# Kernel optimization log

Hardware: AMD Instinct MI355X
Metric: run time of the kernel (lower is better)

## Reference

```python
import jax, jax.numpy as jnp
import numpy as np

R = 3                      # corr_radius
K = (2 * R + 1) ** 2       # 49 correlation window
BANDS = 16
MAX_FREQ = 512.0
NUM_ITERS = 4
EPS = 1e-5


def _fourier(coords):
    # coords [..., D] -> [..., D*(2*BANDS+1)]
    freqs = (2.0 ** jnp.linspace(0.0, np.log2(MAX_FREQ), BANDS).astype(coords.dtype)) * np.pi
    x = coords[..., None] * freqs                      # [..., D, BANDS]
    enc = jnp.concatenate([jnp.sin(x), jnp.cos(x)], axis=-1)
    enc = enc.reshape(enc.shape[:-2] + (-1,))
    return jnp.concatenate([coords, enc], axis=-1)


def _layernorm(x, g, b):
    m = jnp.mean(x, -1, keepdims=True)
    v = jnp.mean(jnp.square(x - m), -1, keepdims=True)
    return (x - m) * jax.lax.rsqrt(v + EPS) * g + b


def _local_corr(query, fmaps, positions, stride):
    # query [B,Q,C], fmaps [B,T,C,H,W], positions [B,Q,T,2] -> corr [B,Q,T,K]
    B, T, C, H, W = fmaps.shape
    Q = query.shape[1]
    off = jnp.arange(-R, R + 1, dtype=positions.dtype)
    oy, ox = jnp.meshgrid(off, off, indexing='ij')
    og = jnp.stack([ox.reshape(-1), oy.reshape(-1)], -1)          # [K,2] (x,y)
    coords = positions / stride
    coords = coords[..., None, :] + og                             # [B,Q,T,K,2]
    coords = jnp.transpose(coords, (0, 2, 1, 3, 4)).reshape(B * T, Q * K, 2)
    fm = fmaps.reshape(B * T, C, H * W)

    def bilerp(f, xy):  # f [C,HW], xy [N,2] -> [C,N]; zeros padding, align_corners=True
        x, y = xy[:, 0], xy[:, 1]
        x0, y0 = jnp.floor(x), jnp.floor(y)
        dx, dy = x - x0, y - y0
        out = jnp.zeros((C, xy.shape[0]), f.dtype)
        for xi, yi, w in ((x0, y0, (1 - dx) * (1 - dy)),
                          (x0 + 1, y0, dx * (1 - dy)),
                          (x0, y0 + 1, (1 - dx) * dy),
                          (x0 + 1, y0 + 1, dx * dy)):
            valid = (xi >= 0) & (xi <= W - 1) & (yi >= 0) & (yi <= H - 1)
            idx = (jnp.clip(yi, 0, H - 1) * W + jnp.clip(xi, 0, W - 1)).astype(jnp.int32)
            out = out + (w * valid)[None, :] * f[:, idx]
        return out

    sampled = jax.vmap(bilerp)(fm, coords)                         # [BT,C,QK]
    sampled = sampled.reshape(B, T, C, Q, K)
    return jnp.einsum('btcqk,bqc->bqtk', sampled, query)


def _forward(coarse_tracks, query_features, feature_maps, feature_stride,
             proj_w, proj_b, ln1_g, ln1_b, conv_w, conv_b, ln2_g, ln2_b,
             mlp_w1, mlp_b1, mlp_w2, mlp_b2, delta_w, delta_b,
             vis_w1, vis_b1, vis_w2, vis_b2):
    B, Q, T, _ = coarse_tracks.shape
    D = proj_w.shape[1]
    dtype = coarse_tracks.dtype
    tracks = coarse_tracks
    t_idx = jnp.linspace(0.0, 1.0, T, dtype=dtype).reshape(1, 1, T, 1)
    hidden = jnp.zeros((B * Q, T, D), dtype)
    vis_sum = jnp.zeros((B, Q, T), dtype)
    num_blocks = ln1_g.shape[0]
    pad = conv_w.shape[-1] // 2
    for _ in range(NUM_ITERS):
        corr = _local_corr(query_features, feature_maps, tracks, feature_stride)
        pos_in = jnp.concatenate([tracks, jnp.broadcast_to(t_idx, (B, Q, T, 1))], -1)
        pos_enc = _fourier(pos_in)
        x = jnp.concatenate([corr, pos_enc, hidden.reshape(B, Q, T, D)], -1)
        x = x.reshape(B * Q, T, -1) @ proj_w + proj_b
        for i in range(num_blocks):
            h = _layernorm(x, ln1_g[i], ln1_b[i])
            h = jnp.transpose(h, (0, 2, 1))                        # [BQ,D,T]
            h = jax.lax.conv_general_dilated(
                h, conv_w[i], (1,), [(pad, pad)],
                dimension_numbers=('NCH', 'OIH', 'NCH'),
                feature_group_count=D) + conv_b[i][None, :, None]
            x = x + jnp.transpose(h, (0, 2, 1))
            h2 = _layernorm(x, ln2_g[i], ln2_b[i])
            x = x + jax.nn.gelu(h2 @ mlp_w1[i] + mlp_b1[i], approximate=False) @ mlp_w2[i] + mlp_b2[i]
        hidden = x
        delta = (x @ delta_w + delta_b).reshape(B, Q, T, 2)
        vis = (jax.nn.gelu(x @ vis_w1 + vis_b1, approximate=False) @ vis_w2 + vis_b2).reshape(B, Q, T)
        tracks = tracks + delta
        vis_sum = vis_sum + vis
    visibility = vis_sum / NUM_ITERS
    return jnp.concatenate([tracks, visibility[..., None]], -1)   # [B,Q,T,3]


def setup_inputs() -> dict:
    B, Q, T, C, H, W, D = 1, 128, 48, 64, 96, 128, 128
    NB, KSZ, IN_DIM = 4, 5, K + 3 * (2 * BANDS + 1) + D          # 49+99+128=276
    ks = jax.random.split(jax.random.key(0), 16)
    s = 0.05
    return {
        'coarse_tracks': jax.random.uniform(ks[0], (B, Q, T, 2)) * jnp.array([W * 4.0, H * 4.0]),
        'query_features': jax.random.normal(ks[1], (B, Q, C)),
        'feature_maps': jax.random.normal(ks[2], (B, T, C, H, W)),
        'feature_stride': 4,
        'proj_w': jax.random.normal(ks[3], (IN_DIM, D)) * s,
        'proj_b': jnp.zeros((D,)),
        'ln1_g': jnp.ones((NB, D)),
        'ln1_b': jnp.zeros((NB, D)),
        'conv_w': jax.random.normal(ks[4], (NB, D, 1, KSZ)) * 0.2,
        'conv_b': jnp.zeros((NB, D)),
        'ln2_g': jnp.ones((NB, D)),
        'ln2_b': jnp.zeros((NB, D)),
        'mlp_w1': jax.random.normal(ks[5], (NB, D, 2 * D)) * s,
        'mlp_b1': jnp.zeros((NB, 2 * D)),
        'mlp_w2': jax.random.normal(ks[6], (NB, 2 * D, D)) * s,
        'mlp_b2': jnp.zeros((NB, D)),
        'delta_w': jax.random.normal(ks[7], (D, 2)) * 0.01,
        'delta_b': jnp.zeros((2,)),
        'vis_w1': jax.random.normal(ks[8], (D, D // 2)) * s,
        'vis_b1': jnp.zeros((D // 2,)),
        'vis_w2': jax.random.normal(ks[9], (D // 2, 1)) * s,
        'vis_b2': jnp.zeros((1,)),
    }


def reference(coarse_tracks, query_features, feature_maps, feature_stride,
              proj_w, proj_b, ln1_g, ln1_b, conv_w, conv_b, ln2_g, ln2_b,
              mlp_w1, mlp_b1, mlp_w2, mlp_b2, delta_w, delta_b,
              vis_w1, vis_b1, vis_w2, vis_b2):
    return _forward(coarse_tracks, query_features, feature_maps, feature_stride,
                    proj_w, proj_b, ln1_g, ln1_b, conv_w, conv_b, ln2_g, ln2_b,
                    mlp_w1, mlp_b1, mlp_w2, mlp_b2, delta_w, delta_b,
                    vis_w1, vis_b1, vis_w2, vis_b2)
```

## Files before the change

kernel.cpp:

```cpp
#include <hip/hip_runtime.h>
#include <hip/hip_bf16.h>
#include <math.h>

#define QN 128
#define TN 48
#define CN 64
#define HN 96
#define WN 128
#define DN 128
#define KK 49
#define IN_DIM 276
#define XPAD 288
#define NROWS (QN*TN)
#define PI_F 3.14159265358979323846f

typedef __hip_bfloat16 bf16;
typedef unsigned short u16;
using bf16x8 = __attribute__((ext_vector_type(8))) short;
using f32x4  = __attribute__((ext_vector_type(4))) float;

__device__ inline float fixnan(float x){ return (x == x && fabsf(x) < 1e30f) ? x : 0.f; }

template<int MODE> __device__ inline float ld(const void* p, size_t i){
  if constexpr (MODE == 0) return ((const float*)p)[i];
  else {
    unsigned int u = ((const unsigned short*)p)[i];
    return __uint_as_float(u << 16);
  }
}

__device__ inline short f2b(float x){
  __hip_bfloat16 h = __float2bfloat16(x);
  return *reinterpret_cast<short*>(&h);
}
__device__ inline float b2f16(u16 u){ return __uint_as_float(((unsigned int)u) << 16); }

__device__ inline float waveReduceSum(float v){
  #pragma unroll
  for (int off = 32; off > 0; off >>= 1) v += __shfl_xor(v, off, 64);
  return v;
}

__device__ inline float gelu_exact(float x){
  return 0.5f * x * (1.f + erff(x * 0.70710678118654752440f));
}

__device__ inline f32x4 mfma16(bf16x8 a, bf16x8 b, f32x4 c){
  return __builtin_amdgcn_mfma_f32_16x16x32_bf16(a, b, c, 0, 0, 0);
}

__device__ inline float decode_stride(const void* p){
  int iv = *(const int*)p;
  if (iv >= 1 && iv <= (1 << 20)) return (float)iv;
  float fv = __int_as_float(iv);
  if (fv == fv && fv >= 0.25f && fv <= 1048576.f) return fv;
  unsigned int lo = ((unsigned int)(*(const unsigned short*)p)) << 16;
  float bv = __uint_as_float(lo);
  if (bv == bv && bv >= 0.25f && bv <= 1048576.f) return bv;
  return 4.f;
}

__device__ inline void bput(short* base, int stride_sh, int r, int k, float v){
  *(short*)((char*)base + (size_t)r*stride_sh*2 + ((2*k) ^ ((r & 7) << 4))) = f2b(v);
}
__device__ inline float bget(const short* base, int stride_sh, int r, int k){
  unsigned short u = *(const unsigned short*)((const char*)base + (size_t)r*stride_sh*2 + ((2*k) ^ ((r & 7) << 4)));
  return __uint_as_float(((unsigned int)u) << 16);
}
__device__ inline bf16x8 bget8(const short* base, int stride_sh, int r, int k0){
  return *(const bf16x8*)((const char*)base + (size_t)r*stride_sh*2 + ((2*k0) ^ ((r & 7) << 4)));
}

struct SLds {
  float sc0[32], sc1[32];
  float hdl[32][132];
  union {
    short Xs[32][320];
    struct { short hn[32][128]; short y1[32][256]; } b;
  } u;
};

__global__ __launch_bounds__(256) void k_sniff(const unsigned short* __restrict__ q,
                                               int* __restrict__ flag){
  __shared__ int cnt;
  if (threadIdx.x == 0) cnt = 0;
  __syncthreads();
  int good = 0;
  for (int i = threadIdx.x; i < 8192; i += 256){
    float v = __uint_as_float(((unsigned int)q[i]) << 16);
    float a = fabsf(v);
    if (a > 1e-3f && a < 30.f) good++;
  }
  atomicAdd(&cnt, good);
  __syncthreads();
  if (threadIdx.x == 0) flag[0] = (cnt > 6500) ? 1 : 0;
}

template<int MODE>
__device__ void transpose_impl(u16 (*tile)[130], const void* fmap, u16* fmapT){
  int t = blockIdx.x / HN, y = blockIdx.x % HN;
  int tid = threadIdx.x, wv = tid >> 6, lane = tid & 63;
  #pragma unroll 4
  for (int ci = 0; ci < 16; ++ci){
    int c = ci*4 + wv;
    size_t base = (((size_t)t*CN + c)*HN + y)*WN;
    if constexpr (MODE == 1){
      const u16* fp = (const u16*)fmap + base + 2*lane;
      tile[c][2*lane]   = fp[0];
      tile[c][2*lane+1] = fp[1];
    } else {
      const float* fp = (const float*)fmap + base + 2*lane;
      tile[c][2*lane]   = (u16)f2b(fp[0]);
      tile[c][2*lane+1] = (u16)f2b(fp[1]);
    }
  }
  __syncthreads();
  u16* op = fmapT + (((size_t)t*HN + y)*WN)*CN + lane;
  #pragma unroll 4
  for (int xi = 0; xi < 32; ++xi){
    int x = xi*4 + wv;
    op[(size_t)x*CN] = tile[lane][x];
  }
}
__global__ __launch_bounds__(256) void k_transpose(const int* __restrict__ mf,
    const void* fmap, u16* fmapT){
  __shared__ u16 tile[64][130];
  if (mf[0] == 0) transpose_impl<0>(tile, fmap, fmapT);
  else            transpose_impl<1>(tile, fmap, fmapT);
}

#define TW_PW   (128*XPAD)
#define TW_W1   (4*256*128)
#define TW_W2   (4*128*256)
#define TW_VW1  (64*128)
#define TW_TOT  (TW_PW + TW_W1 + TW_W2 + TW_VW1)
template<int MODE>
__device__ void transW_impl(int idx, const void* pw, const void* w1, const void* w2,
                            const void* vw1,
                            bf16* pwt, bf16* w1t, bf16* w2t, bf16* vw1t){
  if (idx < TW_PW){
    int n = idx / XPAD, kk = idx % XPAD;
    float v = (kk < IN_DIM) ? ld<MODE>(pw, (size_t)kk*DN + n) : 0.f;
    ((short*)pwt)[idx] = f2b(v);
  } else if (idx < TW_PW + TW_W1){
    int i2 = idx - TW_PW;
    int k = i2 & 127, n = (i2 >> 7) & 255, l = i2 >> 15;
    ((short*)w1t)[i2] = f2b(ld<MODE>(w1, (size_t)l*32768 + (size_t)k*256 + n));
  } else if (idx < TW_PW + TW_W1 + TW_W2){
    int i3 = idx - TW_PW - TW_W1;
    int k = i3 & 255, n = (i3 >> 8) & 127, l = i3 >> 15;
    ((short*)w2t)[i3] = f2b(ld<MODE>(w2, (size_t)l*32768 + (size_t)k*128 + n));
  } else {
    int i4 = idx - TW_PW - TW_W1 - TW_W2;
    int n = i4 >> 7, k = i4 & 127;
    ((short*)vw1t)[i4] = f2b(ld<MODE>(vw1, (size_t)k*64 + n));
  }
}
__global__ __launch_bounds__(256) void k_transW(const int* __restrict__ mf,
    const void* pw, const void* w1, const void* w2, const void* vw1,
    bf16* pwt, bf16* w1t, bf16* w2t, bf16* vw1t){
  int idx = blockIdx.x*256 + threadIdx.x;
  if (idx >= TW_TOT) return;
  if (mf[0] == 0) transW_impl<0>(idx, pw, w1, w2, vw1, pwt, w1t, w2t, vw1t);
  else            transW_impl<1>(idx, pw, w1, w2, vw1, pwt, w1t, w2t, vw1t);
}

template<int MODE>
__device__ void init_impl(const void* ct, float* tracks, float* vis_sum){
  int i = blockIdx.x * 256 + threadIdx.x;
  if (i < NROWS){
    tracks[2*i]   = fixnan(ld<MODE>(ct, 2*i));
    tracks[2*i+1] = fixnan(ld<MODE>(ct, 2*i+1));
    vis_sum[i] = 0.f;
  }
}
__global__ __launch_bounds__(256) void k_init(const int* __restrict__ mf,
    const void* ct, float* tracks, float* vis_sum){
  if (mf[0] == 0) init_impl<0>(ct, tracks, vis_sum);
  else            init_impl<1>(ct, tracks, vis_sum);
}

template<int MODE, int FAST>
__device__ void corr_impl(float* qv, float* dots,
    const void* fmap, const u16* fmapT, const void* query, const void* stride_p,
    const float* __restrict__ tr, short* __restrict__ Xc)
{
  int blk = blockIdx.x;
  int q = blk / TN, t = blk % TN;
  int ll = threadIdx.x;
  qv[ll] = ld<MODE>(query, q*CN + ll);
  float fs = decode_stride(stride_p);
  float c0 = fixnan(tr[2*blk]), c1 = fixnan(tr[2*blk+1]);
  float px = fminf(fmaxf(c0 / fs, -1e6f), 1e6f);
  float py = fminf(fmaxf(c1 / fs, -1e6f), 1e6f);
  float fx0 = floorf(px), fy0 = floorf(py);
  float dx = px - fx0, dy = py - fy0;
  __syncthreads();

  if constexpr (FAST){
    float qv8[8];
    #pragma unroll
    for (int u = 0; u < 8; ++u) qv8[u] = qv[(ll & 7)*8 + u];
    int x0 = (int)fx0 - 3, y0 = (int)fy0 - 3;
    dots[ll] = 0.f;
    __syncthreads();
    if (x0 <= 127 && x0 + 7 >= 0){
      int x0c = min(max(x0, 0), WN - 8);
      int sh = x0c - x0;
      int ip = ll >> 3;
      int i = ip + sh;
      bool wr = ((ll & 7) == 0) && (i >= 0) && (i < 8);
      #pragma unroll
      for (int j = 0; j < 8; ++j){
        int yj = y0 + j;
        if (yj < 0 || yj >= HN) continue;
        const u16* blkp = fmapT + ((((size_t)t*HN + yj)*WN + x0c) << 6);
        bf16x8 v = *(const bf16x8*)(blkp + ll*8);
        float p = 0.f;
        #pragma unroll
        for (int u = 0; u < 8; ++u) p += qv8[u] * b2f16((u16)v[u]);
        p += __shfl_xor(p, 1, 64);
        p += __shfl_xor(p, 2, 64);
        p += __shfl_xor(p, 4, 64);
        if (wr) dots[j*8 + i] = p;
      }
    }
  } else {
    int bx = (int)fx0, by = (int)fy0;
    int j = ll >> 3, i = ll & 7;
    int xi = bx + i - 3, yi = by + j - 3;
    float dot = 0.f;
    if (xi >= 0 && xi < WN && yi >= 0 && yi < HN){
      size_t base = ((size_t)t*CN)*HN*WN + (size_t)yi*WN + xi;
      #pragma unroll 8
      for (int c = 0; c < CN; ++c)
        dot += qv[c] * ld<MODE>(fmap, base + (size_t)c*HN*WN);
    }
    dots[j*8 + i] = dot;
  }
  __syncthreads();

  if (ll < KK){
    int oy = ll / 7, ox = ll % 7;
    float v = (1.f-dx)*(1.f-dy)*dots[oy*8+ox]   + dx*(1.f-dy)*dots[oy*8+ox+1]
            + (1.f-dx)*dy*dots[(oy+1)*8+ox]     + dx*dy*dots[(oy+1)*8+ox+1];
    Xc[(size_t)blk*64 + ll] = f2b(fixnan(v));
  }
}
template<int FAST>
__global__ __launch_bounds__(64) void k_corr(const int* __restrict__ mf,
    const void* fmap, const u16* fmapT, const void* query, const void* stride_p,
    const float* tr, short* Xc)
{
  __shared__ float qv[CN];
  __shared__ float dots[64];
  if (mf[0] == 0) corr_impl<0, FAST>(qv, dots, fmap, fmapT, query, stride_p, tr, Xc);
  else            corr_impl<1, FAST>(qv, dots, fmap, fmapT, query, stride_p, tr, Xc);
}

template<int MODE>
__device__ void iter_impl(SLds& s,
    const short* __restrict__ Xc,
    const float* __restrict__ tr_in, float* __restrict__ tr_out,
    const float* __restrict__ vi_in, float* __restrict__ vi_out,
    const float* __restrict__ hd_in, float* __restrict__ hd_out,
    const bf16* pwt, const void* pb,
    const void* ln1g, const void* ln1b, const void* cw, const void* cb,
    const void* ln2g, const void* ln2b,
    const bf16* w1t, const void* b1, const bf16* w2t, const void* b2,
    const void* dwp, const void* dbp,
    const bf16* vw1t, const void* vb1, const void* vw2, const void* vb2,
    void* out, int last)
{
  int bid = blockIdx.x;
  int q = bid >> 1, half = bid & 1, T0 = half * 16;
  int tid = threadIdx.x, wv = tid >> 6, ll = tid & 63;
  int R0 = q*TN + T0;

  if (tid < 32){
    s.sc0[tid] = fixnan(tr_in[2*(R0 + tid)]);
    s.sc1[tid] = fixnan(tr_in[2*(R0 + tid) + 1]);
  }
  __syncthreads();

  for (int idx = tid; idx < 32*KK; idx += 1024){
    int r = idx / KK, kk = idx % KK;
    bput(&s.u.Xs[0][0], 320, r, kk, b2f16((u16)Xc[(size_t)(R0 + r)*64 + kk]));
  }
  for (int idx = tid; idx < 32*3; idx += 1024){
    int r = idx / 3, cd = idx % 3;
    float v = (cd == 0) ? s.sc0[r] : (cd == 1 ? s.sc1[r] : (float)(T0+r)/(float)(TN-1));
    bput(&s.u.Xs[0][0], 320, r, KK + cd, v);
  }
  for (int idx = tid; idx < 32*96; idx += 1024){
    int r = idx / 96, j = idx % 96, coord = j >> 5, rm = j & 31, band = rm & 15;
    float cv = (coord == 0) ? s.sc0[r] : (coord == 1 ? s.sc1[r] : (float)(T0+r)/(float)(TN-1));
    float a = cv * exp2f(0.6f*(float)band) * PI_F;
    float v = (rm < 16) ? __sinf(a) : __cosf(a);
    bput(&s.u.Xs[0][0], 320, r, KK + 3 + coord*32 + rm, fixnan(v));
  }
  for (int idx = tid; idx < 32*32; idx += 1024){
    int r = idx >> 5, d4 = (idx & 31)*4;
    f32x4 hv = *(const f32x4*)(hd_in + (size_t)(R0 + r)*DN + d4);
    #pragma unroll
    for (int u = 0; u < 4; ++u)
      bput(&s.u.Xs[0][0], 320, r, 148 + d4 + u, fixnan(hv[u]));
  }
  for (int idx = tid; idx < 32*12; idx += 1024){
    int r = idx / 12, p = idx % 12;
    bput(&s.u.Xs[0][0], 320, r, IN_DIM + p, 0.f);
  }
  __syncthreads();

  {
    int rA = ll & 15, gK = ll >> 4;
    int rt = wv & 1, nt = wv >> 1;
    bf16x8 afr[9];
    #pragma unroll
    for (int ks = 0; ks < 9; ++ks)
      afr[ks] = bget8(&s.u.Xs[0][0], 320, rt*16 + rA, ks*32 + gK*8);
    float bv = ld<MODE>(pb, nt*16 + rA);
    f32x4 acc = {bv, bv, bv, bv};
    #pragma unroll
    for (int ks = 0; ks < 9; ++ks)
      acc = mfma16(afr[ks],
        *(const bf16x8*)((const short*)pwt + (size_t)(nt*16 + rA)*XPAD + ks*32 + gK*8), acc);
    #pragma unroll
    for (int r2 = 0; r2 < 4; ++r2)
      s.hdl[rt*16 + gK*4 + r2][nt*16 + rA] = fixnan(acc[r2]);
  }

  int dconv = tid & 127;
  #pragma unroll 1
  for (int L = 0; L < 4; ++L){
    float cwr[5];
    #pragma unroll
    for (int k = 0; k < 5; ++k) cwr[k] = ld<MODE>(cw, ((size_t)L*DN + dconv)*5 + k);
    float cbv = ld<MODE>(cb, L*DN + dconv);
    __syncthreads();
    {
      float g0 = ld<MODE>(ln1g, L*DN + ll), g1 = ld<MODE>(ln1g, L*DN + ll + 64);
      float b0 = ld<MODE>(ln1b, L*DN + ll), b1v = ld<MODE>(ln1b, L*DN + ll + 64);
      #pragma unroll
      for (int rr = 0; rr < 2; ++rr){
        int r = wv*2 + rr;
        float a0 = s.hdl[r][ll], a1 = s.hdl[r][ll+64];
        float su = waveReduceSum(a0 + a1);
        float sq = waveReduceSum(a0*a0 + a1*a1);
        float m = su * (1.f/128.f);
        float var = fmaxf(sq * (1.f/128.f) - m*m, 0.f);
        float inv = rsqrtf(var + 1e-5f);
        bput(&s.u.b.hn[0][0], 128, r, ll,      (a0 - m)*inv*g0 + b0);
        bput(&s.u.b.hn[0][0], 128, r, ll + 64, (a1 - m)*inv*g1 + b1v);
      }
    }
    __syncthreads();
    for (int idx = tid; idx < 32*DN; idx += 1024){
      int r = idx >> 7, t = T0 + r;
      float acc = cbv;
      #pragma unroll
      for (int k = 0; k < 5; ++k){
        int tg = t + k - 2, tl = r + k - 2;
        if (tg >= 0 && tg < TN && tl >= 0 && tl < 32)
          acc += bget(&s.u.b.hn[0][0], 128, tl, dconv) * cwr[k];
      }
      s.hdl[r][dconv] = fixnan(s.hdl[r][dconv] + acc);
    }
    __syncthreads();
    {
      float g0 = ld<MODE>(ln2g, L*DN + ll), g1 = ld<MODE>(ln2g, L*DN + ll + 64);
      float b0 = ld<MODE>(ln2b, L*DN + ll), b1v = ld<MODE>(ln2b, L*DN + ll + 64);
      #pragma unroll
      for (int rr = 0; rr < 2; ++rr){
        int r = wv*2 + rr;
        float a0 = s.hdl[r][ll], a1 = s.hdl[r][ll+64];
        float su = waveReduceSum(a0 + a1);
        float sq = waveReduceSum(a0*a0 + a1*a1);
        float m = su * (1.f/128.f);
        float var = fmaxf(sq * (1.f/128.f) - m*m, 0.f);
        float inv = rsqrtf(var + 1e-5f);
        bput(&s.u.b.hn[0][0], 128, r, ll,      (a0 - m)*inv*g0 + b0);
        bput(&s.u.b.hn[0][0], 128, r, ll + 64, (a1 - m)*inv*g1 + b1v);
      }
    }
    __syncthreads();
    {
      int rA = ll & 15, gK = ll >> 4;
      int rt = wv & 1, nt0 = wv >> 1;
      const short* w1s = (const short*)w1t + (size_t)L*32768;
      bf16x8 afr[4];
      #pragma unroll
      for (int ks = 0; ks < 4; ++ks)
        afr[ks] = bget8(&s.u.b.hn[0][0], 128, rt*16 + rA, ks*32 + gK*8);
      #pragma unroll
      for (int h = 0; h < 2; ++h){
        int nt = nt0 + h*8;
        float bv = ld<MODE>(b1, L*256 + nt*16 + rA);
        f32x4 acc = {bv, bv, bv, bv};
        #pragma unroll
        for (int ks = 0; ks < 4; ++ks)
          acc = mfma16(afr[ks],
            *(const bf16x8*)(w1s + (size_t)(nt*16 + rA)*DN + ks*32 + gK*8), acc);
        #pragma unroll
        for (int r2 = 0; r2 < 4; ++r2)
          bput(&s.u.b.y1[0][0], 256, rt*16 + gK*4 + r2, nt*16 + rA, gelu_exact(acc[r2]));
      }
    }
    __syncthreads();
    {
      int rA = ll & 15, gK = ll >> 4;
      int rt = wv & 1, nt = wv >> 1;
      const short* w2s = (const short*)w2t + (size_t)L*32768;
      bf16x8 afr[8];
      #pragma unroll
      for (int ks = 0; ks < 8; ++ks)
        afr[ks] = bget8(&s.u.b.y1[0][0], 256, rt*16 + rA, ks*32 + gK*8);
      float bv = ld<MODE>(b2, L*DN + nt*16 + rA);
      f32x4 acc = {bv, bv, bv, bv};
      #pragma unroll
      for (int ks = 0; ks < 8; ++ks)
        acc = mfma16(afr[ks],
          *(const bf16x8*)(w2s + (size_t)(nt*16 + rA)*256 + ks*32 + gK*8), acc);
      #pragma unroll
      for (int r2 = 0; r2 < 4; ++r2){
        int r = rt*16 + gK*4 + r2, cc = nt*16 + rA;
        s.hdl[r][cc] = fixnan(s.hdl[r][cc] + acc[r2]);
      }
    }
  }
  __syncthreads();

  for (int idx = tid; idx < 32*DN; idx += 1024){
    int r = idx >> 7, d = idx & 127;
    bput(&s.u.b.hn[0][0], 128, r, d, s.hdl[r][d]);
  }
  __syncthreads();
  float* gC = (float*)&s.u.b.y1[0][0];
  {
    int rA = ll & 15, gK = ll >> 4;
    int rt = wv & 1, nt = wv >> 1;
    if (nt < 4){
      float bv = ld<MODE>(vb1, nt*16 + rA);
      f32x4 acc = {bv, bv, bv, bv};
      #pragma unroll
      for (int ks = 0; ks < 4; ++ks)
        acc = mfma16(bget8(&s.u.b.hn[0][0], 128, rt*16 + rA, ks*32 + gK*8),
                     *(const bf16x8*)((const short*)vw1t + (size_t)(nt*16 + rA)*128 + ks*32 + gK*8), acc);
      #pragma unroll
      for (int r2 = 0; r2 < 4; ++r2)
        gC[(rt*16 + gK*4 + r2)*72 + nt*16 + rA] = gelu_exact(acc[r2]);
    }
  }
  __syncthreads();
  float vw2v = ld<MODE>(vw2, ll);
  float dwa = ld<MODE>(dwp, ll*2),     dwb = ld<MODE>(dwp, (ll+64)*2);
  float dwc = ld<MODE>(dwp, ll*2 + 1), dwd = ld<MODE>(dwp, (ll+64)*2 + 1);
  #pragma unroll
  for (int rr = 0; rr < 2; ++rr){
    int r = wv*2 + rr, t = T0 + r, grow = q*TN + t;
    bool owned = half ? (r >= 8) : (r < 24);
    float vis = waveReduceSum(gC[r*72 + ll] * vw2v);
    float x0 = s.hdl[r][ll], x1 = s.hdl[r][ll+64];
    float dX = waveReduceSum(x0*dwa + x1*dwb);
    float dY = waveReduceSum(x0*dwc + x1*dwd);
    if (owned){
      hd_out[(size_t)grow*DN + ll]      = fixnan(x0);
      hd_out[(size_t)grow*DN + ll + 64] = fixnan(x1);
      if (ll == 0){
        float tx = fixnan(tr_in[2*grow]   + dX + ld<MODE>(dbp, 0));
        float ty = fixnan(tr_in[2*grow+1] + dY + ld<MODE>(dbp, 1));
        tr_out[2*grow] = tx; tr_out[2*grow+1] = ty;
        float vs = fixnan(vi_in[grow] + vis + ld<MODE>(vb2, 0));
        vi_out[grow] = vs;
        if (last){
          if constexpr (MODE == 0){
            ((float*)out)[grow*3 + 0] = tx;
            ((float*)out)[grow*3 + 1] = ty;
            ((float*)out)[grow*3 + 2] = vs * 0.25f;
          } else {
            ((bf16*)out)[grow*3 + 0] = __float2bfloat16(tx);
            ((bf16*)out)[grow*3 + 1] = __float2bfloat16(ty);
            ((bf16*)out)[grow*3 + 2] = __float2bfloat16(vs * 0.25f);
          }
        }
      }
    }
  }
}

__global__ __launch_bounds__(1024, 1) void k_iter(const int* __restrict__ mf,
    const short* Xc,
    const float* tr_in, float* tr_out, const float* vi_in, float* vi_out,
    const float* hd_in, float* hd_out,
    const bf16* pwt, const void* pb,
    const void* ln1g, const void* ln1b, const void* cw, const void* cb,
    const void* ln2g, const void* ln2b,
    const bf16* w1t, const void* b1, const bf16* w2t, const void* b2,
    const void* dwp, const void* dbp,
    const bf16* vw1t, const void* vb1, const void* vw2, const void* vb2,
    void* out, int last)
{
  __shared__ SLds s;
  if (mf[0] == 0)
    iter_impl<0>(s, Xc, tr_in, tr_out, vi_in, vi_out, hd_in, hd_out,
                 pwt, pb, ln1g, ln1b, cw, cb, ln2g, ln2b, w1t, b1, w2t, b2,
                 dwp, dbp, vw1t, vb1, vw2, vb2, out, last);
  else
    iter_impl<1>(s, Xc, tr_in, tr_out, vi_in, vi_out, hd_in, hd_out,
                 pwt, pb, ln1g, ln1b, cw, cb, ln2g, ln2b, w1t, b1, w2t, b2,
                 dwp, dbp, vw1t, vb1, vw2, vb2, out, last);
}

extern "C" void kernel_launch(void* const* d_in, const int* in_sizes, int n_in,
                              void* d_out, int out_size, void* d_ws, size_t ws_size,
                              hipStream_t stream) {
  const void* ct    = d_in[0];
  const void* query = d_in[1];
  const void* fmap  = d_in[2];
  const void* fs    = d_in[3];
  const void* pw    = d_in[4];
  const void* pb    = d_in[5];
  const void* ln1g  = d_in[6];
  const void* ln1b  = d_in[7];
  const void* cw    = d_in[8];
  const void* cb    = d_in[9];
  const void* ln2g  = d_in[10];
  const void* ln2b  = d_in[11];
  const void* w1    = d_in[12];
  const void* b1    = d_in[13];
  const void* w2    = d_in[14];
  const void* b2    = d_in[15];
  const void* dw    = d_in[16];
  const void* db    = d_in[17];
  const void* vw1   = d_in[18];
  const void* vb1   = d_in[19];
  const void* vw2   = d_in[20];
  const void* vb2   = d_in[21];

  char* w0 = (char*)d_ws;
  char* w = w0;
  int*   mflag = (int*)w;                   w += 256;
  float* tr[2]; float* vi[2]; float* hd[2];
  for (int i = 0; i < 2; ++i){ tr[i] = (float*)w; w += ((size_t)NROWS*2*4 + 255) & ~255ull; }
  for (int i = 0; i < 2; ++i){ vi[i] = (float*)w; w += ((size_t)NROWS*4   + 255) & ~255ull; }
  for (int i = 0; i < 2; ++i){ hd[i] = (float*)w; w += ((size_t)NROWS*DN*4 + 255) & ~255ull; }
  short* Xc = (short*)w;                    w += ((size_t)NROWS*64*2 + 255) & ~255ull;
  bf16* pwt = (bf16*)w;                     w += ((size_t)128*XPAD*2 + 255) & ~255ull;
  bf16* w1t = (bf16*)w;                     w += ((size_t)4*256*128*2 + 255) & ~255ull;
  bf16* w2t = (bf16*)w;                     w += ((size_t)4*128*256*2 + 255) & ~255ull;
  bf16* vw1t = (bf16*)w;                    w += ((size_t)64*128*2 + 255) & ~255ull;
  u16*  fmapT = (u16*)w;                    w += ((size_t)TN*HN*WN*CN*2 + 255) & ~255ull;

  bool fast = ((size_t)(w - w0) <= ws_size);

  k_sniff<<<1, 256, 0, stream>>>((const unsigned short*)query, mflag);
  hipMemsetAsync(hd[0], 0, (size_t)NROWS*DN*4, stream);

  k_transW<<<(TW_TOT + 255)/256, 256, 0, stream>>>(mflag, pw, w1, w2, vw1, pwt, w1t, w2t, vw1t);
  k_init<<<(NROWS + 255)/256, 256, 0, stream>>>(mflag, ct, tr[0], vi[0]);
  if (fast)
    k_transpose<<<TN*HN, 256, 0, stream>>>(mflag, fmap, fmapT);

  for (int it = 0; it < 4; ++it){
    int a = it & 1, b = a ^ 1;
    if (fast)
      k_corr<1><<<NROWS, 64, 0, stream>>>(mflag, fmap, fmapT, query, fs, tr[a], Xc);
    else
      k_corr<0><<<NROWS, 64, 0, stream>>>(mflag, fmap, fmapT, query, fs, tr[a], Xc);
    k_iter<<<256, 1024, 0, stream>>>(mflag, Xc,
        tr[a], tr[b], vi[a], vi[b], hd[a], hd[b],
        pwt, pb, ln1g, ln1b, cw, cb, ln2g, ln2b,
        w1t, b1, w2t, b2, dw, db, vw1t, vb1, vw2, vb2,
        d_out, it == 3);
  }
}
```

Before: 324.3 us.

## Fuse next-iteration correlation sampling into the iteration kernel tail

```diff
diff --git a/kernel.cpp b/kernel.cpp
--- a/kernel.cpp
+++ b/kernel.cpp
@@ -73,10 +73,12 @@
 
 struct SLds {
   float sc0[32], sc1[32];
+  float qv[CN];
   float hdl[32][132];
   union {
     short Xs[32][320];
-    struct { short hn[32][128]; short y1[32][256]; } b;
+    struct { short hn[32][128]; short hn2[32][128]; short y1[32][256]; } b;
+    float dots[32][64];
   } u;
 };
 
@@ -166,18 +168,19 @@
 }
 
 template<int MODE>
-__device__ void init_impl(const void* ct, float* tracks, float* vis_sum){
+__device__ void init_impl(const void* ct, float* tracks, float* vis_sum, float* hd0){
   int i = blockIdx.x * 256 + threadIdx.x;
   if (i < NROWS){
     tracks[2*i]   = fixnan(ld<MODE>(ct, 2*i));
     tracks[2*i+1] = fixnan(ld<MODE>(ct, 2*i+1));
     vis_sum[i] = 0.f;
   }
+  if (i < NROWS*DN) hd0[i] = 0.f;
 }
 __global__ __launch_bounds__(256) void k_init(const int* __restrict__ mf,
-    const void* ct, float* tracks, float* vis_sum){
-  if (mf[0] == 0) init_impl<0>(ct, tracks, vis_sum);
-  else            init_impl<1>(ct, tracks, vis_sum);
+    const void* ct, float* tracks, float* vis_sum, float* hd0){
+  if (mf[0] == 0) init_impl<0>(ct, tracks, vis_sum, hd0);
+  else            init_impl<1>(ct, tracks, vis_sum, hd0);
 }
 
 template<int MODE, int FAST>
@@ -207,8 +210,7 @@
     if (x0 <= 127 && x0 + 7 >= 0){
       int x0c = min(max(x0, 0), WN - 8);
       int sh = x0c - x0;
-      int ip = ll >> 3;
-      int i = ip + sh;
+      int i = (ll >> 3) + sh;
       bool wr = ((ll & 7) == 0) && (i >= 0) && (i < 8);
       #pragma unroll
       for (int j = 0; j < 8; ++j){
@@ -258,9 +260,10 @@
   else            corr_impl<1, FAST>(qv, dots, fmap, fmapT, query, stride_p, tr, Xc);
 }
 
-template<int MODE>
+template<int MODE, int TAIL>
 __device__ void iter_impl(SLds& s,
-    const short* __restrict__ Xc,
+    const u16* __restrict__ fmapT, const void* query, const void* stride_p,
+    const short* __restrict__ XcR, short* __restrict__ XcW,
     const float* __restrict__ tr_in, float* __restrict__ tr_out,
     const float* __restrict__ vi_in, float* __restrict__ vi_out,
     const float* __restrict__ hd_in, float* __restrict__ hd_out,
@@ -276,16 +279,18 @@
   int q = bid >> 1, half = bid & 1, T0 = half * 16;
   int tid = threadIdx.x, wv = tid >> 6, ll = tid & 63;
   int R0 = q*TN + T0;
+  float fs = decode_stride(stride_p);
 
   if (tid < 32){
     s.sc0[tid] = fixnan(tr_in[2*(R0 + tid)]);
     s.sc1[tid] = fixnan(tr_in[2*(R0 + tid) + 1]);
   }
+  if (tid >= 64 && tid < 128) s.qv[tid - 64] = ld<MODE>(query, q*CN + (tid - 64));
   __syncthreads();
 
   for (int idx = tid; idx < 32*KK; idx += 1024){
     int r = idx / KK, kk = idx % KK;
-    bput(&s.u.Xs[0][0], 320, r, kk, b2f16((u16)Xc[(size_t)(R0 + r)*64 + kk]));
+    bput(&s.u.Xs[0][0], 320, r, kk, b2f16((u16)XcR[(size_t)(R0 + r)*64 + kk]));
   }
   for (int idx = tid; idx < 32*3; idx += 1024){
     int r = idx / 3, cd = idx % 3;
@@ -330,13 +335,17 @@
       s.hdl[rt*16 + gK*4 + r2][nt*16 + rA] = fixnan(acc[r2]);
   }
 
-  int dconv = tid & 127;
   #pragma unroll 1
   for (int L = 0; L < 4; ++L){
-    float cwr[5];
+    float cwr0[5], cwr1[5];
     #pragma unroll
-    for (int k = 0; k < 5; ++k) cwr[k] = ld<MODE>(cw, ((size_t)L*DN + dconv)*5 + k);
-    float cbv = ld<MODE>(cb, L*DN + dconv);
+    for (int k = 0; k < 5; ++k){
+      cwr0[k] = ld<MODE>(cw, ((size_t)L*DN + ll)*5 + k);
+      cwr1[k] = ld<MODE>(cw, ((size_t)L*DN + ll + 64)*5 + k);
+    }
+    float cbv0 = ld<MODE>(cb, L*DN + ll), cbv1 = ld<MODE>(cb, L*DN + ll + 64);
+    float g20 = ld<MODE>(ln2g, L*DN + ll), g21 = ld<MODE>(ln2g, L*DN + ll + 64);
+    float c20 = ld<MODE>(ln2b, L*DN + ll), c21 = ld<MODE>(ln2b, L*DN + ll + 64);
     __syncthreads();
     {
       float g0 = ld<MODE>(ln1g, L*DN + ll), g1 = ld<MODE>(ln1g, L*DN + ll + 64);
@@ -355,33 +364,28 @@
       }
     }
     __syncthreads();
-    for (int idx = tid; idx < 32*DN; idx += 1024){
-      int r = idx >> 7, t = T0 + r;
-      float acc = cbv;
+    #pragma unroll
+    for (int rr = 0; rr < 2; ++rr){
+      int r = wv*2 + rr, t = T0 + r;
+      float a0 = cbv0, a1 = cbv1;
       #pragma unroll
       for (int k = 0; k < 5; ++k){
         int tg = t + k - 2, tl = r + k - 2;
-        if (tg >= 0 && tg < TN && tl >= 0 && tl < 32)
-          acc += bget(&s.u.b.hn[0][0], 128, tl, dconv) * cwr[k];
+        if (tg >= 0 && tg < TN && tl >= 0 && tl < 32){
+          a0 += bget(&s.u.b.hn[0][0], 128, tl, ll)      * cwr0[k];
+          a1 += bget(&s.u.b.hn[0][0], 128, tl, ll + 64) * cwr1[k];
+        }
       }
-      s.hdl[r][dconv] = fixnan(s.hdl[r][dconv] + acc);
-    }
-    __syncthreads();
-    {
-      float g0 = ld<MODE>(ln2g, L*DN + ll), g1 = ld<MODE>(ln2g, L*DN + ll + 64);
-      float b0 = ld<MODE>(ln2b, L*DN + ll), b1v = ld<MODE>(ln2b, L*DN + ll + 64);
-      #pragma unroll
-      for (int rr = 0; rr < 2; ++rr){
-        int r = wv*2 + rr;
-        float a0 = s.hdl[r][ll], a1 = s.hdl[r][ll+64];
-        float su = waveReduceSum(a0 + a1);
-        float sq = waveReduceSum(a0*a0 + a1*a1);
-        float m = su * (1.f/128.f);
-        float var = fmaxf(sq * (1.f/128.f) - m*m, 0.f);
-        float inv = rsqrtf(var + 1e-5f);
-        bput(&s.u.b.hn[0][0], 128, r, ll,      (a0 - m)*inv*g0 + b0);
-        bput(&s.u.b.hn[0][0], 128, r, ll + 64, (a1 - m)*inv*g1 + b1v);
-      }
+      float x0 = fixnan(s.hdl[r][ll] + a0);
+      float x1 = fixnan(s.hdl[r][ll+64] + a1);
+      s.hdl[r][ll] = x0; s.hdl[r][ll+64] = x1;
+      float su = waveReduceSum(x0 + x1);
+      float sq = waveReduceSum(x0*x0 + x1*x1);
+      float m = su * (1.f/128.f);
+      float var = fmaxf(sq * (1.f/128.f) - m*m, 0.f);
+      float inv = rsqrtf(var + 1e-5f);
+      bput(&s.u.b.hn2[0][0], 128, r, ll,      (x0 - m)*inv*g20 + c20);
+      bput(&s.u.b.hn2[0][0], 128, r, ll + 64, (x1 - m)*inv*g21 + c21);
     }
     __syncthreads();
     {
@@ -391,7 +395,7 @@
       bf16x8 afr[4];
       #pragma unroll
       for (int ks = 0; ks < 4; ++ks)
-        afr[ks] = bget8(&s.u.b.hn[0][0], 128, rt*16 + rA, ks*32 + gK*8);
+        afr[ks] = bget8(&s.u.b.hn2[0][0], 128, rt*16 + rA, ks*32 + gK*8);
       #pragma unroll
       for (int h = 0; h < 2; ++h){
         int nt = nt0 + h*8;
@@ -470,6 +474,7 @@
         float tx = fixnan(tr_in[2*grow]   + dX + ld<MODE>(dbp, 0));
         float ty = fixnan(tr_in[2*grow+1] + dY + ld<MODE>(dbp, 1));
         tr_out[2*grow] = tx; tr_out[2*grow+1] = ty;
+        s.sc0[r] = tx; s.sc1[r] = ty;
         float vs = fixnan(vi_in[grow] + vis + ld<MODE>(vb2, 0));
         vi_out[grow] = vs;
         if (last){
@@ -486,10 +491,60 @@
       }
     }
   }
-}
-
+
+  if constexpr (TAIL){
+    if (!last){
+      __syncthreads();
+      float qv8[8];
+      #pragma unroll
+      for (int u = 0; u < 8; ++u) qv8[u] = s.qv[(ll & 7)*8 + u];
+      #pragma unroll
+      for (int rr = 0; rr < 2; ++rr){
+        int r = wv*2 + rr, t = T0 + r, grow = q*TN + t;
+        bool owned = half ? (r >= 8) : (r < 24);
+        if (!owned) continue;
+        float* dots = &s.u.dots[r][0];
+        float px = fminf(fmaxf(s.sc0[r] / fs, -1e6f), 1e6f);
+        float py = fminf(fmaxf(s.sc1[r] / fs, -1e6f), 1e6f);
+        float fx0 = floorf(px), fy0 = floorf(py);
+        float dx = px - fx0, dy = py - fy0;
+        int x0 = (int)fx0 - 3, y0 = (int)fy0 - 3;
+        dots[ll] = 0.f;
+        if (x0 <= 127 && x0 + 7 >= 0){
+          int x0c = min(max(x0, 0), WN - 8);
+          int sh = x0c - x0;
+          int i = (ll >> 3) + sh;
+          bool wr = ((ll & 7) == 0) && (i >= 0) && (i < 8);
+          #pragma unroll
+          for (int j = 0; j < 8; ++j){
+            int yj = y0 + j;
+            if (yj < 0 || yj >= HN) continue;
+            const u16* blkp = fmapT + ((((size_t)t*HN + yj)*WN + x0c) << 6);
+            bf16x8 v = *(const bf16x8*)(blkp + ll*8);
+            float p = 0.f;
+            #pragma unroll
+            for (int u = 0; u < 8; ++u) p += qv8[u] * b2f16((u16)v[u]);
+            p += __shfl_xor(p, 1, 64);
+            p += __shfl_xor(p, 2, 64);
+            p += __shfl_xor(p, 4, 64);
+            if (wr) dots[j*8 + i] = p;
+          }
+        }
+        if (ll < KK){
+          int oy = ll / 7, ox = ll % 7;
+          float v = (1.f-dx)*(1.f-dy)*dots[oy*8+ox]   + dx*(1.f-dy)*dots[oy*8+ox+1]
+                  + (1.f-dx)*dy*dots[(oy+1)*8+ox]     + dx*dy*dots[(oy+1)*8+ox+1];
+          XcW[(size_t)grow*64 + ll] = f2b(fixnan(v));
+        }
+      }
+    }
+  }
+}
+
+template<int TAIL>
 __global__ __launch_bounds__(1024, 1) void k_iter(const int* __restrict__ mf,
-    const short* Xc,
+    const u16* fmapT, const void* query, const void* stride_p,
+    const short* XcR, short* XcW,
     const float* tr_in, float* tr_out, const float* vi_in, float* vi_out,
     const float* hd_in, float* hd_out,
     const bf16* pwt, const void* pb,
@@ -502,12 +557,12 @@
 {
   __shared__ SLds s;
   if (mf[0] == 0)
-    iter_impl<0>(s, Xc, tr_in, tr_out, vi_in, vi_out, hd_in, hd_out,
-                 pwt, pb, ln1g, ln1b, cw, cb, ln2g, ln2b, w1t, b1, w2t, b2,
+    iter_impl<0, TAIL>(s, fmapT, query, stride_p, XcR, XcW, tr_in, tr_out, vi_in, vi_out,
+                 hd_in, hd_out, pwt, pb, ln1g, ln1b, cw, cb, ln2g, ln2b, w1t, b1, w2t, b2,
                  dwp, dbp, vw1t, vb1, vw2, vb2, out, last);
   else
-    iter_impl<1>(s, Xc, tr_in, tr_out, vi_in, vi_out, hd_in, hd_out,
-                 pwt, pb, ln1g, ln1b, cw, cb, ln2g, ln2b, w1t, b1, w2t, b2,
+    iter_impl<1, TAIL>(s, fmapT, query, stride_p, XcR, XcW, tr_in, tr_out, vi_in, vi_out,
+                 hd_in, hd_out, pwt, pb, ln1g, ln1b, cw, cb, ln2g, ln2b, w1t, b1, w2t, b2,
                  dwp, dbp, vw1t, vb1, vw2, vb2, out, last);
 }
 
@@ -540,11 +595,11 @@
   char* w0 = (char*)d_ws;
   char* w = w0;
   int*   mflag = (int*)w;                   w += 256;
-  float* tr[2]; float* vi[2]; float* hd[2];
+  float* tr[2]; float* vi[2]; float* hd[2]; short* Xc[2];
   for (int i = 0; i < 2; ++i){ tr[i] = (float*)w; w += ((size_t)NROWS*2*4 + 255) & ~255ull; }
   for (int i = 0; i < 2; ++i){ vi[i] = (float*)w; w += ((size_t)NROWS*4   + 255) & ~255ull; }
   for (int i = 0; i < 2; ++i){ hd[i] = (float*)w; w += ((size_t)NROWS*DN*4 + 255) & ~255ull; }
-  short* Xc = (short*)w;                    w += ((size_t)NROWS*64*2 + 255) & ~255ull;
+  for (int i = 0; i < 2; ++i){ Xc[i] = (short*)w; w += ((size_t)NROWS*64*2 + 255) & ~255ull; }
   bf16* pwt = (bf16*)w;                     w += ((size_t)128*XPAD*2 + 255) & ~255ull;
   bf16* w1t = (bf16*)w;                     w += ((size_t)4*256*128*2 + 255) & ~255ull;
   bf16* w2t = (bf16*)w;                     w += ((size_t)4*128*256*2 + 255) & ~255ull;
@@ -554,23 +609,30 @@
   bool fast = ((size_t)(w - w0) <= ws_size);
 
   k_sniff<<<1, 256, 0, stream>>>((const unsigned short*)query, mflag);
-  hipMemsetAsync(hd[0], 0, (size_t)NROWS*DN*4, stream);
-
   k_transW<<<(TW_TOT + 255)/256, 256, 0, stream>>>(mflag, pw, w1, w2, vw1, pwt, w1t, w2t, vw1t);
-  k_init<<<(NROWS + 255)/256, 256, 0, stream>>>(mflag, ct, tr[0], vi[0]);
-  if (fast)
+  k_init<<<(NROWS*DN + 255)/256, 256, 0, stream>>>(mflag, ct, tr[0], vi[0], hd[0]);
+  if (fast){
     k_transpose<<<TN*HN, 256, 0, stream>>>(mflag, fmap, fmapT);
-
-  for (int it = 0; it < 4; ++it){
-    int a = it & 1, b = a ^ 1;
-    if (fast)
-      k_corr<1><<<NROWS, 64, 0, stream>>>(mflag, fmap, fmapT, query, fs, tr[a], Xc);
-    else
-      k_corr<0><<<NROWS, 64, 0, stream>>>(mflag, fmap, fmapT, query, fs, tr[a], Xc);
-    k_iter<<<256, 1024, 0, stream>>>(mflag, Xc,
-        tr[a], tr[b], vi[a], vi[b], hd[a], hd[b],
-        pwt, pb, ln1g, ln1b, cw, cb, ln2g, ln2b,
-        w1t, b1, w2t, b2, dw, db, vw1t, vb1, vw2, vb2,
-        d_out, it == 3);
-  }
-}
+    k_corr<1><<<NROWS, 64, 0, stream>>>(mflag, fmap, fmapT, query, fs, tr[0], Xc[0]);
+    for (int it = 0; it < 4; ++it){
+      int a = it & 1, b = a ^ 1;
+      k_iter<1><<<256, 1024, 0, stream>>>(mflag, fmapT, query, fs,
+          Xc[a], Xc[b],
+          tr[a], tr[b], vi[a], vi[b], hd[a], hd[b],
+          pwt, pb, ln1g, ln1b, cw, cb, ln2g, ln2b,
+          w1t, b1, w2t, b2, dw, db, vw1t, vb1, vw2, vb2,
+          d_out, it == 3);
+    }
+  } else {
+    for (int it = 0; it < 4; ++it){
+      int a = it & 1, b = a ^ 1;
+      k_corr<0><<<NROWS, 64, 0, stream>>>(mflag, fmap, fmapT, query, fs, tr[a], Xc[0]);
+      k_iter<0><<<256, 1024, 0, stream>>>(mflag, fmapT, query, fs,
+          Xc[0], Xc[1],
+          tr[a], tr[b], vi[a], vi[b], hd[a], hd[b],
+          pwt, pb, ln1g, ln1b, cw, cb, ln2g, ln2b,
+          w1t, b1, w2t, b2, dw, db, vw1t, vb1, vw2, vb2,
+          d_out, it == 3);
+    }
+  }
+}
```

Measured after the change: 315.9 us. 1.03x faster.
